# Kernel optimization log

Hardware: AMD Instinct MI355X
Metric: run time of the kernel (lower is better)

## Reference

```python
import jax, jax.numpy as jnp
import numpy as np

B, T, D_IN, D_H, R = 64, 512, 1024, 1024, 16
IN_DIMS = (8, 8, 16)    # 8*8*16 = 1024 = input_size (and hidden_size)
OUT_DIMS = (16, 16, 16)  # 16*16*16 = 4096 = 4*hidden_size


def setup_inputs() -> dict:
    key = jax.random.key(0)
    ks = jax.random.split(key, 14)
    s = 0.5 / np.sqrt(R)  # keep TT product well-scaled

    def cores(k):
        k1, k2, k3, k4, k5, k6 = jax.random.split(k, 6)
        i1, i2, i3 = IN_DIMS
        o1, o2, o3 = OUT_DIMS
        return (
            jax.random.normal(k1, (i1, R)) * s,        # rank-1 boundary squeezed
            jax.random.normal(k2, (R, i2, R)) * s,
            jax.random.normal(k3, (R, i3, R)) * s,
            jax.random.normal(k4, (R, o1, R)) * s,
            jax.random.normal(k5, (R, o2, R)) * s,
            jax.random.normal(k6, (R, o3)) * s,        # rank-1 boundary squeezed
        )

    ih = cores(ks[0])
    hh = cores(ks[1])
    return {
        "x": jax.random.normal(ks[2], (B, T, D_IN), dtype=jnp.float32),
        "ih_g1": ih[0], "ih_g2": ih[1], "ih_g3": ih[2],
        "ih_g4": ih[3], "ih_g5": ih[4], "ih_g6": ih[5],
        "hh_g1": hh[0], "hh_g2": hh[1], "hh_g3": hh[2],
        "hh_g4": hh[3], "hh_g5": hh[4], "hh_g6": hh[5],
        "b_ih": jnp.zeros((4 * D_H,), jnp.float32),
        "b_hh": jnp.zeros((4 * D_H,), jnp.float32),
    }


def tt_matvec(x, g1, g2, g3, g4, g5, g6):
    # x: (B, in_features) -> (B, out_features) via TT weight contraction
    b = x.shape[0]
    t = x.reshape(b, *IN_DIMS)                      # (B, i1, i2, i3)
    t = jnp.einsum('bijk,ia->bjka', t, g1)          # contract in-mode 1
    t = jnp.einsum('bjka,ajc->bkc', t, g2)          # contract in-mode 2
    t = jnp.einsum('bkc,ckd->bd', t, g3)            # contract in-mode 3
    t = jnp.einsum('bd,dne->bne', t, g4)            # expand out-mode 1
    t = jnp.einsum('bne,emf->bnmf', t, g5)          # expand out-mode 2
    t = jnp.einsum('bnmf,fp->bnmp', t, g6)          # expand out-mode 3
    return t.reshape(b, -1)


def reference(x, ih_g1, ih_g2, ih_g3, ih_g4, ih_g5, ih_g6,
              hh_g1, hh_g2, hh_g3, hh_g4, hh_g5, hh_g6, b_ih, b_hh):
    ih_cores = (ih_g1, ih_g2, ih_g3, ih_g4, ih_g5, ih_g6)
    hh_cores = (hh_g1, hh_g2, hh_g3, hh_g4, hh_g5, hh_g6)
    batch = x.shape[0]
    h0 = jnp.zeros((batch, D_H), x.dtype)
    c0 = jnp.zeros((batch, D_H), x.dtype)

    # precompute input-to-hidden projections for all timesteps (batched)
    ih_all = tt_matvec(x.reshape(-1, D_IN), *ih_cores).reshape(batch, -1, 4 * D_H) + b_ih
    ih_all = jnp.swapaxes(ih_all, 0, 1)  # (T, B, 4H)

    def step(carry, ih_t):
        h, c = carry
        gates = ih_t + tt_matvec(h, *hh_cores) + b_hh
        i, f, g, o = jnp.split(gates, 4, axis=1)
        c = jax.nn.sigmoid(f) * c + jax.nn.sigmoid(i) * jnp.tanh(g)
        h = jax.nn.sigmoid(o) * jnp.tanh(c)
        return (h, c), h

    (h, c), hs = jax.lax.scan(step, (h0, c0), ih_all)
    output = jnp.swapaxes(hs, 0, 1)  # (B, T, H)
    return output, (h, c)
```

## Files before the change

### kernel.cpp

```cpp
#include <hip/hip_runtime.h>
#include <math.h>

#define NB   64
#define NT   512
#define DH   1024
#define HID_OFF  33554432
#define HC_SZ    65536


typedef float v2f __attribute__((ext_vector_type(2)));

__device__ __forceinline__ v2f mkv2(float a, float b) { v2f r; r.x = a; r.y = b; return r; }

__device__ __forceinline__ void bar_lgkm() {
    asm volatile("s_waitcnt lgkmcnt(0)\n\ts_barrier" ::: "memory");
}

__device__ __forceinline__ float sigm(float x) { return 1.f / (1.f + __expf(-x)); }
__device__ __forceinline__ float tanh_fast(float x) {
    float e = __expf(2.f * x);
    return 1.f - 2.f / (e + 1.f);
}

__global__ __launch_bounds__(256) void k0_build(
    const float* __restrict__ g1a, const float* __restrict__ g2a,
    const float* __restrict__ g3a, const float* __restrict__ g5a,
    const float* __restrict__ g6a,
    const float* __restrict__ g1b, const float* __restrict__ g2b,
    const float* __restrict__ g3b, const float* __restrict__ g5b,
    const float* __restrict__ g6b,
    float* __restrict__ ATa, float* __restrict__ M2a,
    float* __restrict__ ATb, float* __restrict__ M2b)
{
    const float* g1 = blockIdx.x ? g1b : g1a;
    const float* g2 = blockIdx.x ? g2b : g2a;
    const float* g3 = blockIdx.x ? g3b : g3a;
    const float* g5 = blockIdx.x ? g5b : g5a;
    const float* g6 = blockIdx.x ? g6b : g6a;
    float* A_T = blockIdx.x ? ATb : ATa;
    float* M2  = blockIdx.x ? M2b : M2a;

    __shared__ float Lg1[128], Lg2[2048], Lg3[4096], Lg5[4096], Lg6[256], M1[1024];
    int tid = threadIdx.x;
    for (int i = tid; i < 128;  i += 256) Lg1[i] = g1[i];
    for (int i = tid; i < 2048; i += 256) Lg2[i] = g2[i];
    for (int i = tid; i < 4096; i += 256) Lg3[i] = g3[i];
    for (int i = tid; i < 4096; i += 256) Lg5[i] = g5[i];
    for (int i = tid; i < 256;  i += 256) Lg6[i] = g6[i];
    __syncthreads();
    for (int idx = tid; idx < 1024; idx += 256) {
        int i1 = idx >> 7, j = (idx >> 4) & 7, c = idx & 15;
        float s = 0.f;
        for (int a = 0; a < 16; ++a) s += Lg1[i1 * 16 + a] * Lg2[a * 128 + j * 16 + c];
        M1[idx] = s;
    }
    __syncthreads();
    for (int idx = tid; idx < 16384; idx += 256) {
        int d = idx >> 10, i = idx & 1023;
        int i1 = i >> 7, j = (i >> 4) & 7, k = i & 15;
        float s = 0.f;
        for (int c = 0; c < 16; ++c) s += M1[i1 * 128 + j * 16 + c] * Lg3[c * 256 + k * 16 + d];
        A_T[idx] = s;
    }
    for (int idx = tid; idx < 4096; idx += 256) {
        int e = idx >> 8, mp = idx & 255;
        int m = mp >> 4, p = mp & 15;
        float s = 0.f;
        for (int f = 0; f < 16; ++f) s += Lg5[e * 256 + m * 16 + f] * Lg6[f * 16 + p];
        M2[idx] = s;
    }
}

__global__ __launch_bounds__(256) void k0b_whh(
    const float* __restrict__ g4hh, const float* __restrict__ M2hh,
    float* __restrict__ Whh2)
{
    int n = blockIdx.x;
    int mp = threadIdx.x;
    __shared__ float Ls[256];
    Ls[mp] = g4hh[(mp >> 4) * 256 + n * 16 + (mp & 15)];
    float m2loc[16];
    #pragma unroll
    for (int e = 0; e < 16; ++e) m2loc[e] = M2hh[e * 256 + mp];
    __syncthreads();
    float wv[16];
    #pragma unroll
    for (int d = 0; d < 16; ++d) {
        float s = 0.f;
        #pragma unroll
        for (int e = 0; e < 16; ++e) s = fmaf(Ls[d * 16 + e], m2loc[e], s);
        wv[d] = s;
    }
    float4* dst = (float4*)&Whh2[(size_t)(n * 256 + mp) * 16];
    dst[0] = make_float4(wv[0], wv[1], wv[2], wv[3]);
    dst[1] = make_float4(wv[4], wv[5], wv[6], wv[7]);
    dst[2] = make_float4(wv[8], wv[9], wv[10], wv[11]);
    dst[3] = make_float4(wv[12], wv[13], wv[14], wv[15]);
}

__global__ __launch_bounds__(256) void k1_zy(
    const float* __restrict__ x, const float* __restrict__ A_T,
    const float* __restrict__ g4, float* __restrict__ y_out)
{
    __shared__ float P[16 * 257];
    __shared__ float Q[256];
    __shared__ __align__(16) float Zf[16];
    int tid = threadIdx.x;

    v2f av[4][8];
    #pragma unroll
    for (int j = 0; j < 4; ++j)
        #pragma unroll
        for (int k = 0; k < 8; ++k)
            av[j][k] = mkv2(A_T[(2 * k) * 1024 + tid * 4 + j],
                            A_T[(2 * k + 1) * 1024 + tid * 4 + j]);

    float g4r[16];
    #pragma unroll
    for (int d = 0; d < 16; ++d) g4r[d] = g4[d * 256 + tid];

    int row0 = blockIdx.x * 16;
    float4 xv = *(const float4*)&x[(size_t)row0 * 1024 + tid * 4];
    for (int r = 0; r < 16; ++r) {
        int row = row0 + r;
        v2f pd[8];
        #pragma unroll
        for (int k = 0; k < 8; ++k) {
            v2f acc = xv.x * av[0][k];
            acc += xv.y * av[1][k];
            acc += xv.z * av[2][k];
            acc += xv.w * av[3][k];
            pd[k] = acc;
        }
        #pragma unroll
        for (int k = 0; k < 8; ++k) {
            P[(2 * k) * 257 + tid]     = pd[k].x;
            P[(2 * k + 1) * 257 + tid] = pd[k].y;
        }
        if (r < 15)
            xv = *(const float4*)&x[(size_t)(row + 1) * 1024 + tid * 4];
        bar_lgkm();
        {
            int d = tid & 15, s = tid >> 4;
            float v = 0.f;
            #pragma unroll
            for (int j2 = 0; j2 < 16; ++j2) v += P[d * 257 + s * 16 + j2];
            Q[d * 16 + s] = v;
        }
        bar_lgkm();
        if (tid < 16) {
            float v = 0.f;
            #pragma unroll
            for (int s2 = 0; s2 < 16; ++s2) v += Q[tid * 16 + s2];
            Zf[tid] = v;
        }
        bar_lgkm();
        {
            v2f ya = mkv2(0.f, 0.f);
            const v2f* zf2 = (const v2f*)Zf;
            #pragma unroll
            for (int k = 0; k < 8; ++k) ya += zf2[k] * mkv2(g4r[2 * k], g4r[2 * k + 1]);
            y_out[(size_t)row * 256 + tid] = ya.x + ya.y;
        }
    }
}

__global__ __launch_bounds__(1024) void k2_lstm(
    const float* __restrict__ A_T_hh, const float* __restrict__ Whh2,
    const float* __restrict__ M2ih, const float* __restrict__ y_ih_g,
    const float* __restrict__ b_ih, const float* __restrict__ b_hh,
    float* __restrict__ pfdump, float* __restrict__ out)
{
    __shared__ __align__(16) float Lh[1024];
    __shared__ __align__(16) float Pz[32];

    const int tid  = threadIdx.x;
    const int b    = blockIdx.x;
    const int lane = tid & 63;
    const int w    = tid >> 6;
    const int dg   = w >> 1;
    const int ws   = w & 1;
    const int mp   = tid & 255;
    const int n0   = tid >> 8;
    const int n0u  = __builtin_amdgcn_readfirstlane(n0);

    const int ibase = ws * 512 + lane * 8;
    v2f a0p[4], a1p[4];
    {
        const v2f* a0v = (const v2f*)&A_T_hh[(2 * dg) * 1024 + ibase];
        const v2f* a1v = (const v2f*)&A_T_hh[(2 * dg + 1) * 1024 + ibase];
        #pragma unroll
        for (int k = 0; k < 4; ++k) { a0p[k] = a0v[k]; a1p[k] = a1v[k]; }
    }

    v2f whh[4][8];
    #pragma unroll
    for (int g = 0; g < 4; ++g) {
        const float4* wr4 = (const float4*)&Whh2[(size_t)((n0 + 4 * g) * 256 + mp) * 16];
        float4 f0 = wr4[0], f1 = wr4[1], f2 = wr4[2], f3 = wr4[3];
        whh[g][0] = mkv2(f0.x, f0.y); whh[g][1] = mkv2(f0.z, f0.w);
        whh[g][2] = mkv2(f1.x, f1.y); whh[g][3] = mkv2(f1.z, f1.w);
        whh[g][4] = mkv2(f2.x, f2.y); whh[g][5] = mkv2(f2.z, f2.w);
        whh[g][6] = mkv2(f3.x, f3.y); whh[g][7] = mkv2(f3.z, f3.w);
    }
    float m2i[16];
    #pragma unroll
    for (int e = 0; e < 16; ++e) m2i[e] = M2ih[e * 256 + mp];
    float bias0 = b_ih[tid]        + b_hh[tid];
    float bias1 = b_ih[1024 + tid] + b_hh[1024 + tid];
    float bias2 = b_ih[2048 + tid] + b_hh[2048 + tid];
    float bias3 = b_ih[3072 + tid] + b_hh[3072 + tid];

    Lh[tid] = 0.f;
    float h = 0.f, c = 0.f;
    __syncthreads();

    const float* yrow = y_ih_g + (size_t)b * (NT * 256);
    float*       orow = out + (size_t)b * (NT * 1024);

    for (int t = 0; t < NT; ++t) {
        float p0, p1;
        {
            const v2f* hv2 = (const v2f*)&Lh[ibase];
            v2f hp0 = hv2[0], hp1 = hv2[1], hp2 = hv2[2], hp3 = hv2[3];
            v2f s0 = hp0 * a0p[0]; s0 += hp1 * a0p[1]; s0 += hp2 * a0p[2]; s0 += hp3 * a0p[3];
            v2f s1 = hp0 * a1p[0]; s1 += hp1 * a1p[1]; s1 += hp2 * a1p[2]; s1 += hp3 * a1p[3];
            p0 = s0.x + s0.y;
            p1 = s1.x + s1.y;
        }
        #pragma unroll
        for (int m = 1; m <= 32; m <<= 1) {
            p0 += __shfl_xor(p0, m, 64);
            p1 += __shfl_xor(p1, m, 64);
        }
        if (lane == 0) *(v2f*)&Pz[ws * 16 + 2 * dg] = mkv2(p0, p1);
        bar_lgkm();

        v2f zp[8];
        {
            const float4* pz4 = (const float4*)Pz;
            float4 q0 = pz4[0], q1 = pz4[1], q2 = pz4[2], q3 = pz4[3];
            float4 r0 = pz4[4], r1 = pz4[5], r2 = pz4[6], r3 = pz4[7];
            float4 s0 = make_float4(q0.x + r0.x, q0.y + r0.y, q0.z + r0.z, q0.w + r0.w);
            float4 s1 = make_float4(q1.x + r1.x, q1.y + r1.y, q1.z + r1.z, q1.w + r1.w);
            float4 s2 = make_float4(q2.x + r2.x, q2.y + r2.y, q2.z + r2.z, q2.w + r2.w);
            float4 s3 = make_float4(q3.x + r3.x, q3.y + r3.y, q3.z + r3.z, q3.w + r3.w);
            zp[0] = mkv2(s0.x, s0.y); zp[1] = mkv2(s0.z, s0.w);
            zp[2] = mkv2(s1.x, s1.y); zp[3] = mkv2(s1.z, s1.w);
            zp[4] = mkv2(s2.x, s2.y); zp[5] = mkv2(s2.z, s2.w);
            zp[6] = mkv2(s3.x, s3.y); zp[7] = mkv2(s3.z, s3.w);
        }

        float acc0, acc1, acc2, acc3;
        {
            v2f a0 = zp[0] * whh[0][0], a1 = zp[0] * whh[1][0];
            v2f a2 = zp[0] * whh[2][0], a3 = zp[0] * whh[3][0];
            #pragma unroll
            for (int k = 1; k < 8; ++k) {
                a0 += zp[k] * whh[0][k];
                a1 += zp[k] * whh[1][k];
                a2 += zp[k] * whh[2][k];
                a3 += zp[k] * whh[3][k];
            }
            acc0 = bias0 + a0.x + a0.y;
            acc1 = bias1 + a1.x + a1.y;
            acc2 = bias2 + a2.x + a2.y;
            acc3 = bias3 + a3.x + a3.y;
        }

        {
            const float4* yb4 = (const float4*)(yrow + t * 256);
            #pragma unroll
            for (int g = 0; g < 4; ++g) {
                int base = (n0u + 4 * g) * 4;
                float4 q0 = yb4[base], q1 = yb4[base + 1], q2 = yb4[base + 2], q3 = yb4[base + 3];
                float a = q0.x * m2i[0];
                a = fmaf(q0.y, m2i[1], a);  a = fmaf(q0.z, m2i[2], a);  a = fmaf(q0.w, m2i[3], a);
                a = fmaf(q1.x, m2i[4], a);  a = fmaf(q1.y, m2i[5], a);  a = fmaf(q1.z, m2i[6], a);
                a = fmaf(q1.w, m2i[7], a);  a = fmaf(q2.x, m2i[8], a);  a = fmaf(q2.y, m2i[9], a);
                a = fmaf(q2.z, m2i[10], a); a = fmaf(q2.w, m2i[11], a); a = fmaf(q3.x, m2i[12], a);
                a = fmaf(q3.y, m2i[13], a); a = fmaf(q3.z, m2i[14], a); a = fmaf(q3.w, m2i[15], a);
                if (g == 0) acc0 += a;
                else if (g == 1) acc1 += a;
                else if (g == 2) acc2 += a;
                else acc3 += a;
            }
        }

        float ig = sigm(acc0);
        float fg = sigm(acc1);
        float gg = tanh_fast(acc2);
        float og = sigm(acc3);
        c = fg * c + ig * gg;
        h = og * tanh_fast(c);

        Lh[tid] = h;
        orow[t * 1024 + tid] = h;

        if (tid < 256) {
            int tn = (t + 1 < NT) ? (t + 1) : (NT - 1);
            pfdump[tid] = yrow[tn * 256 + tid];
        }
        bar_lgkm();
    }

    out[HID_OFF + b * 1024 + tid] = h;
    out[HID_OFF + HC_SZ + b * 1024 + tid] = c;
}

extern "C" void kernel_launch(void* const* d_in, const int* in_sizes, int n_in,
                              void* d_out, int out_size, void* d_ws, size_t ws_size,
                              hipStream_t stream) {
    const float* x     = (const float*)d_in[0];
    const float* ihg1  = (const float*)d_in[1];
    const float* ihg2  = (const float*)d_in[2];
    const float* ihg3  = (const float*)d_in[3];
    const float* ihg4  = (const float*)d_in[4];
    const float* ihg5  = (const float*)d_in[5];
    const float* ihg6  = (const float*)d_in[6];
    const float* hhg1  = (const float*)d_in[7];
    const float* hhg2  = (const float*)d_in[8];
    const float* hhg3  = (const float*)d_in[9];
    const float* hhg4  = (const float*)d_in[10];
    const float* hhg5  = (const float*)d_in[11];
    const float* hhg6  = (const float*)d_in[12];
    const float* b_ih  = (const float*)d_in[13];
    const float* b_hh  = (const float*)d_in[14];
    float* out = (float*)d_out;

    float* ws     = (float*)d_ws;
    float* ATih   = ws;
    float* AThh   = ws + 16384;
    float* M2ih   = ws + 32768;
    float* M2hh   = ws + 36864;
    float* Whh2   = ws + 40960;
    float* pfdump = ws + 106496;
    float* yih    = ws + 106752;

    hipLaunchKernelGGL(k0_build, dim3(2), dim3(256), 0, stream,
                       ihg1, ihg2, ihg3, ihg5, ihg6,
                       hhg1, hhg2, hhg3, hhg5, hhg6,
                       ATih, M2ih, AThh, M2hh);
    hipLaunchKernelGGL(k0b_whh, dim3(16), dim3(256), 0, stream,
                       hhg4, M2hh, Whh2);
    hipLaunchKernelGGL(k1_zy, dim3(2048), dim3(256), 0, stream,
                       x, ATih, ihg4, yih);
    hipLaunchKernelGGL(k2_lstm, dim3(NB), dim3(1024), 0, stream,
                       AThh, Whh2, M2ih, yih, b_ih, b_hh, pfdump, out);
}
```

Baseline: 1.684 ms.

## Use DPP wave reductions, restructure input projection, and prefetch y ahead in LSTM loop

Splits the TT core build across more blocks, and rewrites the input projection kernel so each wave reduces its partial sums with DPP instead of multi-stage LDS reductions, processing two row groups per block. The recurrent kernel replaces shuffle-xor reductions with DPP reductions plus LDS atomics into a double-buffered accumulator, which drops the cross-wave merge step. It also loads the y projection for the current step at the start of each iteration and touches y four steps ahead to warm the cache, replacing the previous single-step prefetch. The atomics and extra registers may raise contention or register pressure, and the workspace offset shifts.

```diff
diff --git a/kernel.cpp b/kernel.cpp
--- a/kernel.cpp
+++ b/kernel.cpp
@@ -14,6 +14,21 @@
 
 __device__ __forceinline__ void bar_lgkm() {
     asm volatile("s_waitcnt lgkmcnt(0)\n\ts_barrier" ::: "memory");
+}
+
+template<int CTRL>
+__device__ __forceinline__ float dpp_add(float v) {
+    int m = __builtin_amdgcn_update_dpp(0, __builtin_bit_cast(int, v), CTRL, 0xf, 0xf, true);
+    return v + __builtin_bit_cast(float, m);
+}
+__device__ __forceinline__ float wave_red_sum(float v) {
+    v = dpp_add<0x111>(v);
+    v = dpp_add<0x112>(v);
+    v = dpp_add<0x114>(v);
+    v = dpp_add<0x118>(v);
+    v = dpp_add<0x142>(v);
+    v = dpp_add<0x143>(v);
+    return v;
 }
 
 __device__ __forceinline__ float sigm(float x) { return 1.f / (1.f + __expf(-x)); }
@@ -55,19 +70,22 @@
         M1[idx] = s;
     }
     __syncthreads();
-    for (int idx = tid; idx < 16384; idx += 256) {
+    int base = 4096 * blockIdx.y;
+    for (int idx = base + tid; idx < base + 4096; idx += 256) {
         int d = idx >> 10, i = idx & 1023;
         int i1 = i >> 7, j = (i >> 4) & 7, k = i & 15;
         float s = 0.f;
         for (int c = 0; c < 16; ++c) s += M1[i1 * 128 + j * 16 + c] * Lg3[c * 256 + k * 16 + d];
         A_T[idx] = s;
     }
-    for (int idx = tid; idx < 4096; idx += 256) {
-        int e = idx >> 8, mp = idx & 255;
-        int m = mp >> 4, p = mp & 15;
-        float s = 0.f;
-        for (int f = 0; f < 16; ++f) s += Lg5[e * 256 + m * 16 + f] * Lg6[f * 16 + p];
-        M2[idx] = s;
+    if (blockIdx.y == 0) {
+        for (int idx = tid; idx < 4096; idx += 256) {
+            int e = idx >> 8, mp = idx & 255;
+            int m = mp >> 4, p = mp & 15;
+            float s = 0.f;
+            for (int f = 0; f < 16; ++f) s += Lg5[e * 256 + m * 16 + f] * Lg6[f * 16 + p];
+            M2[idx] = s;
+        }
     }
 }
 
@@ -102,66 +120,84 @@
     const float* __restrict__ x, const float* __restrict__ A_T,
     const float* __restrict__ g4, float* __restrict__ y_out)
 {
-    __shared__ float P[16 * 257];
-    __shared__ float Q[256];
-    __shared__ __align__(16) float Zf[16];
-    int tid = threadIdx.x;
-
-    v2f av[4][8];
-    #pragma unroll
-    for (int j = 0; j < 4; ++j)
-        #pragma unroll
-        for (int k = 0; k < 8; ++k)
-            av[j][k] = mkv2(A_T[(2 * k) * 1024 + tid * 4 + j],
-                            A_T[(2 * k + 1) * 1024 + tid * 4 + j]);
-
-    float g4r[16];
-    #pragma unroll
-    for (int d = 0; d < 16; ++d) g4r[d] = g4[d * 256 + tid];
-
-    int row0 = blockIdx.x * 16;
-    float4 xv = *(const float4*)&x[(size_t)row0 * 1024 + tid * 4];
-    for (int r = 0; r < 16; ++r) {
-        int row = row0 + r;
-        v2f pd[8];
-        #pragma unroll
-        for (int k = 0; k < 8; ++k) {
-            v2f acc = xv.x * av[0][k];
-            acc += xv.y * av[1][k];
-            acc += xv.z * av[2][k];
-            acc += xv.w * av[3][k];
-            pd[k] = acc;
-        }
-        #pragma unroll
-        for (int k = 0; k < 8; ++k) {
-            P[(2 * k) * 257 + tid]     = pd[k].x;
-            P[(2 * k + 1) * 257 + tid] = pd[k].y;
-        }
-        if (r < 15)
-            xv = *(const float4*)&x[(size_t)(row + 1) * 1024 + tid * 4];
+    __shared__ __align__(16) float Z[2][2][2][16];
+
+    const int tid  = threadIdx.x;
+    const int lane = tid & 63;
+    const int w    = tid >> 6;
+    const int s    = w >> 1;
+    const int wp   = w & 1;
+    const int i0   = wp * 512 + lane * 8;
+
+    v2f av[8][8];
+    #pragma unroll
+    for (int d = 0; d < 16; ++d) {
+        float Ar[8];
+        *(float4*)&Ar[0] = *(const float4*)&A_T[d * 1024 + i0];
+        *(float4*)&Ar[4] = *(const float4*)&A_T[d * 1024 + i0 + 4];
+        #pragma unroll
+        for (int ip = 0; ip < 8; ++ip) {
+            if (d & 1) av[ip][d >> 1].y = Ar[ip];
+            else       av[ip][d >> 1].x = Ar[ip];
+        }
+    }
+    const int u0 = wp * 128 + lane;
+    const int u1 = u0 + 64;
+    float g4r0[16], g4r1[16];
+    #pragma unroll
+    for (int d = 0; d < 16; ++d) {
+        g4r0[d] = g4[d * 256 + u0];
+        g4r1[d] = g4[d * 256 + u1];
+    }
+
+    const int rbase = (blockIdx.x * 2 + s) * 16;
+    float xr[8];
+    *(float4*)&xr[0] = *(const float4*)&x[(size_t)rbase * 1024 + i0];
+    *(float4*)&xr[4] = *(const float4*)&x[(size_t)rbase * 1024 + i0 + 4];
+
+    for (int rr = 0; rr < 16; ++rr) {
+        const int row = rbase + rr;
+        const int rp  = rr & 1;
+        float xn[8];
+        if (rr < 15) {
+            *(float4*)&xn[0] = *(const float4*)&x[(size_t)(row + 1) * 1024 + i0];
+            *(float4*)&xn[4] = *(const float4*)&x[(size_t)(row + 1) * 1024 + i0 + 4];
+        }
+        v2f p[8];
+        #pragma unroll
+        for (int dd = 0; dd < 8; ++dd) p[dd] = xr[0] * av[0][dd];
+        #pragma unroll
+        for (int ip = 1; ip < 8; ++ip)
+            #pragma unroll
+            for (int dd = 0; dd < 8; ++dd) p[dd] += xr[ip] * av[ip][dd];
+        #pragma unroll
+        for (int dd = 0; dd < 8; ++dd) {
+            float sx = wave_red_sum(p[dd].x);
+            float sy = wave_red_sum(p[dd].y);
+            if (lane == 63) *(v2f*)&Z[s][rp][wp][2 * dd] = mkv2(sx, sy);
+        }
         bar_lgkm();
-        {
-            int d = tid & 15, s = tid >> 4;
-            float v = 0.f;
-            #pragma unroll
-            for (int j2 = 0; j2 < 16; ++j2) v += P[d * 257 + s * 16 + j2];
-            Q[d * 16 + s] = v;
-        }
-        bar_lgkm();
-        if (tid < 16) {
-            float v = 0.f;
-            #pragma unroll
-            for (int s2 = 0; s2 < 16; ++s2) v += Q[tid * 16 + s2];
-            Zf[tid] = v;
-        }
-        bar_lgkm();
-        {
-            v2f ya = mkv2(0.f, 0.f);
-            const v2f* zf2 = (const v2f*)Zf;
-            #pragma unroll
-            for (int k = 0; k < 8; ++k) ya += zf2[k] * mkv2(g4r[2 * k], g4r[2 * k + 1]);
-            y_out[(size_t)row * 256 + tid] = ya.x + ya.y;
-        }
+        float zs[16];
+        {
+            const float4* za = (const float4*)&Z[s][rp][0][0];
+            const float4* zb = (const float4*)&Z[s][rp][1][0];
+            float4 a0 = za[0], a1 = za[1], a2 = za[2], a3 = za[3];
+            float4 b0 = zb[0], b1 = zb[1], b2 = zb[2], b3 = zb[3];
+            *(float4*)&zs[0]  = make_float4(a0.x + b0.x, a0.y + b0.y, a0.z + b0.z, a0.w + b0.w);
+            *(float4*)&zs[4]  = make_float4(a1.x + b1.x, a1.y + b1.y, a1.z + b1.z, a1.w + b1.w);
+            *(float4*)&zs[8]  = make_float4(a2.x + b2.x, a2.y + b2.y, a2.z + b2.z, a2.w + b2.w);
+            *(float4*)&zs[12] = make_float4(a3.x + b3.x, a3.y + b3.y, a3.z + b3.z, a3.w + b3.w);
+        }
+        float y0 = zs[0] * g4r0[0], y1 = zs[0] * g4r1[0];
+        #pragma unroll
+        for (int d = 1; d < 16; ++d) {
+            y0 = fmaf(zs[d], g4r0[d], y0);
+            y1 = fmaf(zs[d], g4r1[d], y1);
+        }
+        y_out[(size_t)row * 256 + u0] = y0;
+        y_out[(size_t)row * 256 + u1] = y1;
+        #pragma unroll
+        for (int ip = 0; ip < 8; ++ip) xr[ip] = xn[ip];
     }
 }
 
@@ -172,25 +208,23 @@
     float* __restrict__ pfdump, float* __restrict__ out)
 {
     __shared__ __align__(16) float Lh[1024];
-    __shared__ __align__(16) float Pz[32];
+    __shared__ __align__(16) float Lz[2][16];
 
     const int tid  = threadIdx.x;
     const int b    = blockIdx.x;
     const int lane = tid & 63;
     const int w    = tid >> 6;
     const int dg   = w >> 1;
-    const int ws   = w & 1;
+    const int wsl  = w & 1;
     const int mp   = tid & 255;
     const int n0   = tid >> 8;
-    const int n0u  = __builtin_amdgcn_readfirstlane(n0);
-
-    const int ibase = ws * 512 + lane * 8;
+
+    const int ibase = wsl * 512 + 2 * lane;
     v2f a0p[4], a1p[4];
-    {
-        const v2f* a0v = (const v2f*)&A_T_hh[(2 * dg) * 1024 + ibase];
-        const v2f* a1v = (const v2f*)&A_T_hh[(2 * dg + 1) * 1024 + ibase];
-        #pragma unroll
-        for (int k = 0; k < 4; ++k) { a0p[k] = a0v[k]; a1p[k] = a1v[k]; }
+    #pragma unroll
+    for (int k = 0; k < 4; ++k) {
+        a0p[k] = *(const v2f*)&A_T_hh[(2 * dg) * 1024 + ibase + 128 * k];
+        a1p[k] = *(const v2f*)&A_T_hh[(2 * dg + 1) * 1024 + ibase + 128 * k];
     }
 
     v2f whh[4][8];
@@ -212,79 +246,78 @@
     float bias3 = b_ih[3072 + tid] + b_hh[3072 + tid];
 
     Lh[tid] = 0.f;
+    if (tid < 32) ((float*)Lz)[tid] = 0.f;
     float h = 0.f, c = 0.f;
     __syncthreads();
 
     const float* yrow = y_ih_g + (size_t)b * (NT * 256);
     float*       orow = out + (size_t)b * (NT * 1024);
+    float pfacc = 0.f;
 
     for (int t = 0; t < NT; ++t) {
+        const int p = t & 1;
+
+        const int ybase = __builtin_amdgcn_readfirstlane(t * 256 + n0 * 16);
+        float yv[4][16];
+        #pragma unroll
+        for (int g = 0; g < 4; ++g)
+            #pragma unroll
+            for (int e = 0; e < 16; ++e)
+                yv[g][e] = yrow[ybase + g * 64 + e];
+        float ypf = 0.f;
+        {
+            int tpf = (t + 4 < NT) ? (t + 4) : (NT - 1);
+            if (tid < 256) ypf = yrow[tpf * 256 + tid];
+        }
+
         float p0, p1;
         {
             const v2f* hv2 = (const v2f*)&Lh[ibase];
-            v2f hp0 = hv2[0], hp1 = hv2[1], hp2 = hv2[2], hp3 = hv2[3];
+            v2f hp0 = hv2[0], hp1 = hv2[64], hp2 = hv2[128], hp3 = hv2[192];
             v2f s0 = hp0 * a0p[0]; s0 += hp1 * a0p[1]; s0 += hp2 * a0p[2]; s0 += hp3 * a0p[3];
             v2f s1 = hp0 * a1p[0]; s1 += hp1 * a1p[1]; s1 += hp2 * a1p[2]; s1 += hp3 * a1p[3];
             p0 = s0.x + s0.y;
             p1 = s1.x + s1.y;
         }
-        #pragma unroll
-        for (int m = 1; m <= 32; m <<= 1) {
-            p0 += __shfl_xor(p0, m, 64);
-            p1 += __shfl_xor(p1, m, 64);
-        }
-        if (lane == 0) *(v2f*)&Pz[ws * 16 + 2 * dg] = mkv2(p0, p1);
+        p0 = wave_red_sum(p0);
+        p1 = wave_red_sum(p1);
+        if (lane == 63) {
+            atomicAdd(&Lz[p][2 * dg], p0);
+            atomicAdd(&Lz[p][2 * dg + 1], p1);
+        }
         bar_lgkm();
 
-        v2f zp[8];
-        {
-            const float4* pz4 = (const float4*)Pz;
-            float4 q0 = pz4[0], q1 = pz4[1], q2 = pz4[2], q3 = pz4[3];
-            float4 r0 = pz4[4], r1 = pz4[5], r2 = pz4[6], r3 = pz4[7];
-            float4 s0 = make_float4(q0.x + r0.x, q0.y + r0.y, q0.z + r0.z, q0.w + r0.w);
-            float4 s1 = make_float4(q1.x + r1.x, q1.y + r1.y, q1.z + r1.z, q1.w + r1.w);
-            float4 s2 = make_float4(q2.x + r2.x, q2.y + r2.y, q2.z + r2.z, q2.w + r2.w);
-            float4 s3 = make_float4(q3.x + r3.x, q3.y + r3.y, q3.z + r3.z, q3.w + r3.w);
-            zp[0] = mkv2(s0.x, s0.y); zp[1] = mkv2(s0.z, s0.w);
-            zp[2] = mkv2(s1.x, s1.y); zp[3] = mkv2(s1.z, s1.w);
-            zp[4] = mkv2(s2.x, s2.y); zp[5] = mkv2(s2.z, s2.w);
-            zp[6] = mkv2(s3.x, s3.y); zp[7] = mkv2(s3.z, s3.w);
-        }
-
+        float zs[16];
+        {
+            const float4* z4 = (const float4*)&Lz[p][0];
+            *(float4*)&zs[0]  = z4[0];
+            *(float4*)&zs[4]  = z4[1];
+            *(float4*)&zs[8]  = z4[2];
+            *(float4*)&zs[12] = z4[3];
+        }
         float acc0, acc1, acc2, acc3;
         {
-            v2f a0 = zp[0] * whh[0][0], a1 = zp[0] * whh[1][0];
-            v2f a2 = zp[0] * whh[2][0], a3 = zp[0] * whh[3][0];
+            const v2f* zp = (const v2f*)zs;
+            v2f A0 = zp[0] * whh[0][0], A1 = zp[0] * whh[1][0];
+            v2f A2 = zp[0] * whh[2][0], A3 = zp[0] * whh[3][0];
             #pragma unroll
             for (int k = 1; k < 8; ++k) {
-                a0 += zp[k] * whh[0][k];
-                a1 += zp[k] * whh[1][k];
-                a2 += zp[k] * whh[2][k];
-                a3 += zp[k] * whh[3][k];
+                A0 += zp[k] * whh[0][k];
+                A1 += zp[k] * whh[1][k];
+                A2 += zp[k] * whh[2][k];
+                A3 += zp[k] * whh[3][k];
             }
-            acc0 = bias0 + a0.x + a0.y;
-            acc1 = bias1 + a1.x + a1.y;
-            acc2 = bias2 + a2.x + a2.y;
-            acc3 = bias3 + a3.x + a3.y;
-        }
-
-        {
-            const float4* yb4 = (const float4*)(yrow + t * 256);
-            #pragma unroll
-            for (int g = 0; g < 4; ++g) {
-                int base = (n0u + 4 * g) * 4;
-                float4 q0 = yb4[base], q1 = yb4[base + 1], q2 = yb4[base + 2], q3 = yb4[base + 3];
-                float a = q0.x * m2i[0];
-                a = fmaf(q0.y, m2i[1], a);  a = fmaf(q0.z, m2i[2], a);  a = fmaf(q0.w, m2i[3], a);
-                a = fmaf(q1.x, m2i[4], a);  a = fmaf(q1.y, m2i[5], a);  a = fmaf(q1.z, m2i[6], a);
-                a = fmaf(q1.w, m2i[7], a);  a = fmaf(q2.x, m2i[8], a);  a = fmaf(q2.y, m2i[9], a);
-                a = fmaf(q2.z, m2i[10], a); a = fmaf(q2.w, m2i[11], a); a = fmaf(q3.x, m2i[12], a);
-                a = fmaf(q3.y, m2i[13], a); a = fmaf(q3.z, m2i[14], a); a = fmaf(q3.w, m2i[15], a);
-                if (g == 0) acc0 += a;
-                else if (g == 1) acc1 += a;
-                else if (g == 2) acc2 += a;
-                else acc3 += a;
-            }
+            acc0 = bias0 + A0.x + A0.y;
+            acc1 = bias1 + A1.x + A1.y;
+            acc2 = bias2 + A2.x + A2.y;
+            acc3 = bias3 + A3.x + A3.y;
+        }
+        #pragma unroll
+        for (int e = 0; e < 16; ++e) {
+            acc0 = fmaf(yv[0][e], m2i[e], acc0);
+            acc1 = fmaf(yv[1][e], m2i[e], acc1);
+            acc2 = fmaf(yv[2][e], m2i[e], acc2);
+            acc3 = fmaf(yv[3][e], m2i[e], acc3);
         }
 
         float ig = sigm(acc0);
@@ -296,16 +329,14 @@
 
         Lh[tid] = h;
         orow[t * 1024 + tid] = h;
-
-        if (tid < 256) {
-            int tn = (t + 1 < NT) ? (t + 1) : (NT - 1);
-            pfdump[tid] = yrow[tn * 256 + tid];
-        }
+        if (tid < 16) Lz[p ^ 1][tid] = 0.f;
+        pfacc += ypf;
         bar_lgkm();
     }
 
     out[HID_OFF + b * 1024 + tid] = h;
     out[HID_OFF + HC_SZ + b * 1024 + tid] = c;
+    if (tid < 256) pfdump[tid] = pfacc;
 }
 
 extern "C" void kernel_launch(void* const* d_in, const int* in_sizes, int n_in,
@@ -335,15 +366,15 @@
     float* M2hh   = ws + 36864;
     float* Whh2   = ws + 40960;
     float* pfdump = ws + 106496;
-    float* yih    = ws + 106752;
-
-    hipLaunchKernelGGL(k0_build, dim3(2), dim3(256), 0, stream,
+    float* yih    = ws + 107520;
+
+    hipLaunchKernelGGL(k0_build, dim3(2, 4), dim3(256), 0, stream,
                        ihg1, ihg2, ihg3, ihg5, ihg6,
                        hhg1, hhg2, hhg3, hhg5, hhg6,
                        ATih, M2ih, AThh, M2hh);
     hipLaunchKernelGGL(k0b_whh, dim3(16), dim3(256), 0, stream,
                        hhg4, M2hh, Whh2);
-    hipLaunchKernelGGL(k1_zy, dim3(2048), dim3(256), 0, stream,
+    hipLaunchKernelGGL(k1_zy, dim3(1024), dim3(256), 0, stream,
                        x, ATih, ihg4, yih);
     hipLaunchKernelGGL(k2_lstm, dim3(NB), dim3(1024), 0, stream,
                        AThh, Whh2, M2ih, yih, b_ih, b_hh, pfdump, out);
```

New measurement: 1.564 ms. 7.1% less time.
